# Kernel tuning notes

Measured on AMD Instinct MI355X. Metric: run time of the kernel, lower is better.

## Reference

```python
import jax, jax.numpy as jnp
import numpy as np
from jax import lax

EMB_DIM = 16
NUM_EMB = 32
DN = ('NCDHW', 'OIDHW', 'NCDHW')


def conv3d(x, w, b, stride, pad):
    y = lax.conv_general_dilated(x, w, window_strides=(stride,) * 3,
                                 padding=[(pad, pad)] * 3, dimension_numbers=DN)
    return y + b[None, :, None, None, None]


def deconv3d(x, w, b, stride, pad):
    # PyTorch ConvTranspose3d: weight (Cin,Cout,k,k,k); equivalent to conv with
    # spatially flipped, channel-transposed kernel, lhs_dilation=stride, pad=k-1-p.
    k = w.shape[-1]
    wf = jnp.flip(w, axis=(2, 3, 4)).transpose(1, 0, 2, 3, 4)  # (Cout,Cin,k,k,k)
    y = lax.conv_general_dilated(x, wf, window_strides=(1, 1, 1),
                                 padding=[(k - 1 - pad, k - 1 - pad)] * 3,
                                 lhs_dilation=(stride,) * 3, dimension_numbers=DN)
    return y + b[None, :, None, None, None]


def setup_inputs() -> dict:
    key = jax.random.key(0)
    ks = jax.random.split(key, 16)
    x = jax.random.normal(ks[0], (16, 3, 16, 128, 128), dtype=jnp.float32)
    s = 0.05
    # encoder params
    enc_w1 = jax.random.normal(ks[1], (4, 3, 4, 4, 4), jnp.float32) * s
    enc_b1 = jnp.zeros((4,), jnp.float32)
    enc_w2 = jax.random.normal(ks[2], (8, 4, 4, 4, 4), jnp.float32) * s
    enc_b2 = jnp.zeros((8,), jnp.float32)
    enc_w4 = jax.random.normal(ks[3], (EMB_DIM, 8, 3, 3, 3), jnp.float32) * s
    enc_b4 = jnp.zeros((EMB_DIM,), jnp.float32)
    # decoder params (ConvTranspose3d layout: (Cin, Cout, k, k, k))
    dec_w1 = jax.random.normal(ks[4], (EMB_DIM, 8, 4, 4, 4), jnp.float32) * s
    dec_b1 = jnp.zeros((8,), jnp.float32)
    dec_w3 = jax.random.normal(ks[5], (8, 4, 4, 4, 4), jnp.float32) * s
    dec_b3 = jnp.zeros((4,), jnp.float32)
    dec_w4 = jax.random.normal(ks[6], (4, 3, 3, 3, 3), jnp.float32) * s
    dec_b4 = jnp.zeros((3,), jnp.float32)
    # codebook buffers: normalize(randn)*0.1, rows 0/1 forced
    e = jax.random.normal(ks[7], (NUM_EMB, EMB_DIM), jnp.float32)
    e = e / jnp.linalg.norm(e, axis=1, keepdims=True) * 0.1
    embedding = e.at[0].set(0.0).at[1].set(6.0)
    cluster_size = jnp.ones((NUM_EMB,), jnp.float32)
    return dict(x=x, epoch=60,
                enc_w1=enc_w1, enc_b1=enc_b1, enc_w2=enc_w2, enc_b2=enc_b2,
                enc_w4=enc_w4, enc_b4=enc_b4,
                dec_w1=dec_w1, dec_b1=dec_b1, dec_w3=dec_w3, dec_b3=dec_b3,
                dec_w4=dec_w4, dec_b4=dec_b4,
                embedding=embedding, cluster_size=cluster_size)


def reference(x, epoch, enc_w1, enc_b1, enc_w2, enc_b2, enc_w4, enc_b4,
              dec_w1, dec_b1, dec_w3, dec_b3, dec_w4, dec_b4,
              embedding, cluster_size):
    # ---- Encoder ----
    h = jax.nn.relu(conv3d(x, enc_w1, enc_b1, 2, 1))
    h = jax.nn.relu(conv3d(h, enc_w2, enc_b2, 2, 1))
    z = jnp.clip(conv3d(h, enc_w4, enc_b4, 1, 1), 0.0, 6.0)  # relu(relu6(.))
    B, C, Dd, Hh, Ww = z.shape

    # ---- VQ-EMA forward (epoch >= 50 branch) ----
    emb = embedding.at[0].set(0.0).at[1].set(6.0)
    flat = z.transpose(0, 2, 3, 4, 1).reshape(-1, C)  # (N, D)
    # squared euclidean distances; argmin matches cdist argmin
    d2 = (jnp.sum(flat * flat, axis=1, keepdims=True)
          - 2.0 * flat @ emb.T + jnp.sum(emb * emb, axis=1))
    idx = jnp.argmin(d2, axis=1)                       # (N,)
    q = emb[idx]                                       # (N, D)
    quant = q.reshape(B, Dd, Hh, Ww, C).transpose(0, 4, 1, 2, 3)

    N = flat.shape[0]
    avg_probs = jnp.zeros((NUM_EMB,), flat.dtype).at[idx].add(1.0) / N
    perplexity = jnp.exp(-jnp.sum(avg_probs * jnp.log(avg_probs + 1e-10)))
    used_codes = jnp.sum(cluster_size > 1e-5).astype(jnp.float32) / NUM_EMB

    quantized_st = z + lax.stop_gradient(quant - z)
    vq_loss = 0.25 * jnp.mean((lax.stop_gradient(quant) - z) ** 2)
    codes = idx.reshape(B, Dd, Hh, Ww)

    # ---- Decoder ----
    d = jax.nn.relu(deconv3d(quantized_st, dec_w1, dec_b1, 2, 1))
    d = jax.nn.relu(deconv3d(d, dec_w3, dec_b3, 2, 1))
    out = deconv3d(d, dec_w4, dec_b4, 1, 1)
    return out, vq_loss, codes, perplexity, used_codes
```

## Files before the change

kernel.cpp:

```cpp
#include <hip/hip_runtime.h>
#include <math.h>

#define NB 16


__device__ __forceinline__ float4 ld4(const float* p) {
  return *reinterpret_cast<const float4*>(p);
}
__device__ __forceinline__ void st4(float* p, float4 v) {
  *reinterpret_cast<float4*>(p) = v;
}

__global__ __launch_bounds__(256) void conv1_k(
    const float* __restrict__ x, const float* __restrict__ w,
    const float* __restrict__ bias, float* __restrict__ y) {
  int idx = blockIdx.x * 256 + threadIdx.x;
  int g  = idx & 15;
  int oh = (idx >> 4) & 63;
  int od = (idx >> 10) & 7;
  int n  = idx >> 13;
  bool gl = (g > 0), gr = (g < 15);
  float acc[4][4];
  #pragma unroll
  for (int co = 0; co < 4; co++) {
    float bv = bias[co];
    #pragma unroll
    for (int m = 0; m < 4; m++) acc[co][m] = bv;
  }
  int ih0 = 2 * oh - 1;
  #pragma unroll 1
  for (int ci = 0; ci < 3; ci++) {
    #pragma unroll 1
    for (int kd = 0; kd < 4; kd++) {
      int id = 2 * od - 1 + kd;
      bool vd = (unsigned)id < 16u;
      int idc = vd ? id : 0;
      const float* plane = x + (((n * 3 + ci) * 16 + idc) * 16384);
      #pragma unroll
      for (int kh = 0; kh < 4; kh++) {
        int ih = ih0 + kh;
        bool v = vd && ((unsigned)ih < 128u);
        int ihc = (unsigned)ih < 128u ? ih : 0;
        const float* rp = plane + ihc * 128 + 8 * g;
        float r[10];
        float4 A = ld4(rp);
        float4 B = ld4(rp + 4);
        float rl = rp[-1 * (int)gl];
        float rr = rp[gr ? 8 : 0];
        r[0] = (v && gl) ? rl : 0.0f;
        r[1] = v ? A.x : 0.0f; r[2] = v ? A.y : 0.0f;
        r[3] = v ? A.z : 0.0f; r[4] = v ? A.w : 0.0f;
        r[5] = v ? B.x : 0.0f; r[6] = v ? B.y : 0.0f;
        r[7] = v ? B.z : 0.0f; r[8] = v ? B.w : 0.0f;
        r[9] = (v && gr) ? rr : 0.0f;
        #pragma unroll
        for (int co = 0; co < 4; co++) {
          const float* wb = w + ((co * 3 + ci) * 4 + kd) * 16 + kh * 4;
          #pragma unroll
          for (int kw = 0; kw < 4; kw++) {
            float wv = wb[kw];
            #pragma unroll
            for (int m = 0; m < 4; m++)
              acc[co][m] += r[2 * m + kw] * wv;
          }
        }
      }
    }
  }
  #pragma unroll
  for (int co = 0; co < 4; co++) {
    float4 o;
    o.x = fmaxf(acc[co][0], 0.0f); o.y = fmaxf(acc[co][1], 0.0f);
    o.z = fmaxf(acc[co][2], 0.0f); o.w = fmaxf(acc[co][3], 0.0f);
    st4(y + ((n * 4 + co) * 8 + od) * 4096 + oh * 64 + 4 * g, o);
  }
}

__global__ __launch_bounds__(256) void conv2_k(
    const float* __restrict__ y1, const float* __restrict__ w,
    const float* __restrict__ bias, float* __restrict__ y) {
  int idx = blockIdx.x * 256 + threadIdx.x;
  int ow = idx & 31;
  int oh = (idx >> 5) & 31;
  int od = (idx >> 10) & 3;
  int n = (idx >> 12) & 15;
  int cog = idx >> 16;
  float acc[4];
  #pragma unroll
  for (int co = 0; co < 4; co++) acc[co] = bias[cog * 4 + co];
  int id0 = 2 * od - 1, ih0 = 2 * oh - 1, iw0 = 2 * ow - 1;
  bool vh[4], vw[4];
  #pragma unroll
  for (int l = 0; l < 4; l++) {
    vh[l] = (unsigned)(ih0 + l) < 64u;
    vw[l] = (unsigned)(iw0 + l) < 64u;
  }
  #pragma unroll 1
  for (int ci = 0; ci < 4; ci++) {
    const float* ip = y1 + ((n * 4 + ci) * 8) * 4096;
    #pragma unroll
    for (int kd = 0; kd < 4; kd++) {
      int id = id0 + kd;
      bool vd = (unsigned)id < 8u;
      const float* pp = ip + id * 4096;
      float p[4][4];
      #pragma unroll
      for (int kh = 0; kh < 4; kh++)
        #pragma unroll
        for (int kw = 0; kw < 4; kw++)
          p[kh][kw] = (vd && vh[kh] && vw[kw]) ? pp[(ih0 + kh) * 64 + (iw0 + kw)] : 0.0f;
      #pragma unroll
      for (int co = 0; co < 4; co++) {
        const float* wp = w + (((cog * 4 + co) * 4 + ci) * 4 + kd) * 16;
        #pragma unroll
        for (int kh = 0; kh < 4; kh++)
          #pragma unroll
          for (int kw = 0; kw < 4; kw++)
            acc[co] += p[kh][kw] * wp[kh * 4 + kw];
      }
    }
  }
  #pragma unroll
  for (int co = 0; co < 4; co++)
    y[((n * 8 + cog * 4 + co) * 4 + od) * 1024 + oh * 32 + ow] = fmaxf(acc[co], 0.0f);
}

__global__ __launch_bounds__(256) void conv4_k(
    const float* __restrict__ y2, const float* __restrict__ w,
    const float* __restrict__ bias, float* __restrict__ z) {
  int idx = blockIdx.x * 256 + threadIdx.x;
  int ow = idx & 31;
  int oh = (idx >> 5) & 31;
  int od = (idx >> 10) & 3;
  int n = (idx >> 12) & 15;
  int cog = idx >> 16;
  float acc[4];
  #pragma unroll
  for (int co = 0; co < 4; co++) acc[co] = bias[cog * 4 + co];
  bool vh[3], vw[3];
  #pragma unroll
  for (int l = 0; l < 3; l++) {
    vh[l] = (unsigned)(oh - 1 + l) < 32u;
    vw[l] = (unsigned)(ow - 1 + l) < 32u;
  }
  #pragma unroll 1
  for (int ci = 0; ci < 8; ci++) {
    const float* ip = y2 + ((n * 8 + ci) * 4) * 1024;
    #pragma unroll
    for (int kd = 0; kd < 3; kd++) {
      int id = od - 1 + kd;
      bool vd = (unsigned)id < 4u;
      const float* pp = ip + id * 1024;
      float p[3][3];
      #pragma unroll
      for (int kh = 0; kh < 3; kh++)
        #pragma unroll
        for (int kw = 0; kw < 3; kw++)
          p[kh][kw] = (vd && vh[kh] && vw[kw]) ? pp[(oh - 1 + kh) * 32 + (ow - 1 + kw)] : 0.0f;
      #pragma unroll
      for (int co = 0; co < 4; co++) {
        const float* wp = w + (((cog * 4 + co) * 8 + ci) * 3 + kd) * 9;
        #pragma unroll
        for (int kh = 0; kh < 3; kh++)
          #pragma unroll
          for (int kw = 0; kw < 3; kw++)
            acc[co] += p[kh][kw] * wp[kh * 3 + kw];
      }
    }
  }
  #pragma unroll
  for (int co = 0; co < 4; co++)
    z[((n * 16 + cog * 4 + co) * 4 + od) * 1024 + oh * 32 + ow] =
        fminf(fmaxf(acc[co], 0.0f), 6.0f);
}

__global__ __launch_bounds__(256) void vq_k(
    const float* __restrict__ z, const float* __restrict__ emb,
    float* __restrict__ quant, float* __restrict__ codes_out,
    float* __restrict__ stats) {
  __shared__ float se[32 * 16];
  __shared__ float se2[32];
  __shared__ float shist[32];
  __shared__ float swred[4];
  int tid = threadIdx.x;
  for (int i = tid; i < 512; i += 256) {
    int r = i >> 4;
    float v = emb[i];
    if (r == 0) v = 0.0f;
    else if (r == 1) v = 6.0f;
    se[i] = v;
  }
  if (tid < 32) shist[tid] = 0.0f;
  __syncthreads();
  if (tid < 32) {
    float s = 0.0f;
    #pragma unroll
    for (int d = 0; d < 16; d++) { float v = se[tid * 16 + d]; s += v * v; }
    se2[tid] = s;
  }
  __syncthreads();

  int idx = blockIdx.x * 256 + tid;
  float lsum = 0.0f;
  {
    int w_ = idx & 31; int t = idx >> 5;
    int h_ = t & 31; t >>= 5;
    int d_ = t & 3;  int b_ = t >> 2;
    const float* zp = z + b_ * 65536 + d_ * 1024 + h_ * 32 + w_;
    float f[16];
    float f2 = 0.0f;
    #pragma unroll
    for (int c = 0; c < 16; c++) { float v = zp[c * 4096]; f[c] = v; f2 += v * v; }
    float best = 1e30f; int bi = 0;
    for (int e = 0; e < 32; e++) {
      float dot = 0.0f;
      #pragma unroll
      for (int c = 0; c < 16; c++) dot += f[c] * se[e * 16 + c];
      float d2 = f2 - 2.0f * dot + se2[e];
      if (d2 < best) { best = d2; bi = e; }
    }
    float* qp = quant + b_ * 65536 + d_ * 1024 + h_ * 32 + w_;
    #pragma unroll
    for (int c = 0; c < 16; c++) {
      float q = se[bi * 16 + c];
      qp[c * 4096] = q;
      float df = q - f[c];
      lsum += df * df;
    }
    codes_out[idx] = (float)bi;
    atomicAdd(&shist[bi], 1.0f);
  }
  for (int o = 32; o; o >>= 1) lsum += __shfl_down(lsum, o);
  if ((tid & 63) == 0) swred[tid >> 6] = lsum;
  __syncthreads();
  if (tid == 0) atomicAdd(&stats[0], swred[0] + swred[1] + swred[2] + swred[3]);
  if (tid < 32) {
    float h = shist[tid];
    if (h != 0.0f) atomicAdd(&stats[1 + tid], h);
  }
}

__global__ void init_stats_k(float* __restrict__ stats) {
  int tid = threadIdx.x;
  if (tid < 33) stats[tid] = 0.0f;
}

__global__ void fin_k(const float* __restrict__ stats,
                      const float* __restrict__ cluster_size,
                      float* __restrict__ out_loss, float* __restrict__ out_perp,
                      float* __restrict__ out_used) {
  int tid = threadIdx.x;
  float v = 0.0f;
  float used = 0.0f;
  if (tid < 32) {
    float p = stats[1 + tid] * (1.0f / 65536.0f);
    v = p * logf(p + 1e-10f);
    used = (cluster_size[tid] > 1e-5f) ? 1.0f : 0.0f;
  }
  for (int o = 16; o; o >>= 1) { v += __shfl_down(v, o); used += __shfl_down(used, o); }
  if (tid == 0) {
    *out_perp = expf(-v);
    *out_used = used * (1.0f / 32.0f);
    *out_loss = 0.25f * stats[0] * (1.0f / 1048576.0f);
  }
}

__global__ __launch_bounds__(256) void deconv1_k(
    const float* __restrict__ q, const float* __restrict__ w,
    const float* __restrict__ bias, float* __restrict__ d1) {
  int bid = blockIdx.x;
  int cog = bid & 1;
  int ph  = (bid >> 1) & 1;
  int od  = (bid >> 2) & 7;
  int n   = bid >> 5;
  int tid = threadIdx.x;
  int g   = tid & 7;
  int bl  = tid >> 3;
  bool glf = (g > 0), grf = (g < 7);

  int kd0 = (od + 1) & 1;
  int idtop = (od + 1 - kd0) >> 1;
  int kh0 = (ph + 1) & 1;
  int ihtop = bl + ph;

  float acc[4][8];
  #pragma unroll
  for (int co = 0; co < 4; co++) {
    float bv = bias[cog * 4 + co];
    #pragma unroll
    for (int m = 0; m < 8; m++) acc[co][m] = bv;
  }

  #pragma unroll 1
  for (int ci = 0; ci < 16; ci++) {
    const float* ip = q + ((n * 16 + ci) * 4) * 1024;
    #pragma unroll
    for (int jd = 0; jd < 2; jd++) {
      int id = idtop - jd;
      bool vd = (unsigned)id < 4u;
      int idc = vd ? id : 0;
      const float* plane = ip + idc * 1024;
      #pragma unroll
      for (int jh = 0; jh < 2; jh++) {
        int ih = ihtop - jh;
        bool v = vd && ((unsigned)ih < 32u);
        int ihc = (unsigned)ih < 32u ? ih : 0;
        const float* rp = plane + ihc * 32 + 4 * g;
        float r[6];
        float4 A = ld4(rp);
        float rl = rp[-1 * (int)glf];
        float rr = rp[grf ? 4 : 0];
        r[0] = (v && glf) ? rl : 0.0f;
        r[1] = v ? A.x : 0.0f; r[2] = v ? A.y : 0.0f;
        r[3] = v ? A.z : 0.0f; r[4] = v ? A.w : 0.0f;
        r[5] = (v && grf) ? rr : 0.0f;
        int kd = kd0 + 2 * jd;
        int kh = kh0 + 2 * jh;
        #pragma unroll
        for (int co = 0; co < 4; co++) {
          const float* wb = w + ((ci * 8 + cog * 4 + co) * 4 + kd) * 16 + kh * 4;
          #pragma unroll
          for (int jw = 0; jw < 2; jw++) {
            float w_ev = wb[1 + 2 * jw];
            float w_od = wb[2 * jw];
            #pragma unroll
            for (int ii = 0; ii < 4; ii++) {
              acc[co][2 * ii]     += r[ii + 1 - jw] * w_ev;
              acc[co][2 * ii + 1] += r[ii + 2 - jw] * w_od;
            }
          }
        }
      }
    }
  }
  int oh = 2 * bl + ph;
  #pragma unroll
  for (int co = 0; co < 4; co++) {
    float* op = d1 + ((n * 8 + cog * 4 + co) * 8 + od) * 4096 + oh * 64 + 8 * g;
    float4 lo, hi;
    lo.x = fmaxf(acc[co][0], 0.0f); lo.y = fmaxf(acc[co][1], 0.0f);
    lo.z = fmaxf(acc[co][2], 0.0f); lo.w = fmaxf(acc[co][3], 0.0f);
    hi.x = fmaxf(acc[co][4], 0.0f); hi.y = fmaxf(acc[co][5], 0.0f);
    hi.z = fmaxf(acc[co][6], 0.0f); hi.w = fmaxf(acc[co][7], 0.0f);
    st4(op, lo); st4(op + 4, hi);
  }
}

__global__ __launch_bounds__(256) void deconv3_k(
    const float* __restrict__ d1, const float* __restrict__ w,
    const float* __restrict__ bias, float* __restrict__ d2) {
  int bid = blockIdx.x;
  int ph  = bid & 1;
  int blh = (bid >> 1) & 3;
  int od  = (bid >> 3) & 15;
  int n   = bid >> 7;
  int tid = threadIdx.x;
  int g   = tid & 15;
  int bl  = tid >> 4;
  int BL  = blh * 16 + bl;
  bool glf = (g > 0), grf = (g < 15);

  int kd0 = (od + 1) & 1;
  int idtop = (od + 1 - kd0) >> 1;
  int kh0 = (ph + 1) & 1;
  int ihtop = BL + ph;

  float acc[4][8];
  #pragma unroll
  for (int co = 0; co < 4; co++) {
    float bv = bias[co];
    #pragma unroll
    for (int m = 0; m < 8; m++) acc[co][m] = bv;
  }

  #pragma unroll 1
  for (int ci = 0; ci < 8; ci++) {
    const float* ip = d1 + ((n * 8 + ci) * 8) * 4096;
    #pragma unroll
    for (int jd = 0; jd < 2; jd++) {
      int id = idtop - jd;
      bool vd = (unsigned)id < 8u;
      int idc = vd ? id : 0;
      const float* plane = ip + idc * 4096;
      #pragma unroll
      for (int jh = 0; jh < 2; jh++) {
        int ih = ihtop - jh;
        bool v = vd && ((unsigned)ih < 64u);
        int ihc = (unsigned)ih < 64u ? ih : 0;
        const float* rp = plane + ihc * 64 + 4 * g;
        float r[6];
        float4 A = ld4(rp);
        float rl = rp[-1 * (int)glf];
        float rr = rp[grf ? 4 : 0];
        r[0] = (v && glf) ? rl : 0.0f;
        r[1] = v ? A.x : 0.0f; r[2] = v ? A.y : 0.0f;
        r[3] = v ? A.z : 0.0f; r[4] = v ? A.w : 0.0f;
        r[5] = (v && grf) ? rr : 0.0f;
        int kd = kd0 + 2 * jd;
        int kh = kh0 + 2 * jh;
        #pragma unroll
        for (int co = 0; co < 4; co++) {
          const float* wb = w + ((ci * 4 + co) * 4 + kd) * 16 + kh * 4;
          #pragma unroll
          for (int jw = 0; jw < 2; jw++) {
            float w_ev = wb[1 + 2 * jw];
            float w_od = wb[2 * jw];
            #pragma unroll
            for (int ii = 0; ii < 4; ii++) {
              acc[co][2 * ii]     += r[ii + 1 - jw] * w_ev;
              acc[co][2 * ii + 1] += r[ii + 2 - jw] * w_od;
            }
          }
        }
      }
    }
  }
  int oh = 2 * BL + ph;
  #pragma unroll
  for (int co = 0; co < 4; co++) {
    float* op = d2 + ((n * 4 + co) * 16 + od) * 16384 + oh * 128 + 8 * g;
    float4 lo, hi;
    lo.x = fmaxf(acc[co][0], 0.0f); lo.y = fmaxf(acc[co][1], 0.0f);
    lo.z = fmaxf(acc[co][2], 0.0f); lo.w = fmaxf(acc[co][3], 0.0f);
    hi.x = fmaxf(acc[co][4], 0.0f); hi.y = fmaxf(acc[co][5], 0.0f);
    hi.z = fmaxf(acc[co][6], 0.0f); hi.w = fmaxf(acc[co][7], 0.0f);
    st4(op, lo); st4(op + 4, hi);
  }
}

__global__ __launch_bounds__(256) void deconv4_k(
    const float* __restrict__ d2, const float* __restrict__ w,
    const float* __restrict__ bias, float* __restrict__ out) {
  int idx = blockIdx.x * 256 + threadIdx.x;
  int g  = idx & 15;
  int oh = (idx >> 4) & 127;
  int od = (idx >> 11) & 15;
  int n  = idx >> 15;
  bool gl = (g > 0), gr = (g < 15);
  float acc[3][8];
  #pragma unroll
  for (int co = 0; co < 3; co++) {
    float bv = bias[co];
    #pragma unroll
    for (int m = 0; m < 8; m++) acc[co][m] = bv;
  }
  int ih0 = oh - 1;
  #pragma unroll 1
  for (int ci = 0; ci < 4; ci++) {
    const float* ip = d2 + ((n * 4 + ci) * 16) * 16384;
    #pragma unroll
    for (int kd = 0; kd < 3; kd++) {
      int id = od - 1 + kd;
      bool vd = (unsigned)id < 16u;
      int idc = vd ? id : 0;
      const float* plane = ip + idc * 16384;
      #pragma unroll
      for (int kh = 0; kh < 3; kh++) {
        int ih = ih0 + kh;
        bool v = vd && ((unsigned)ih < 128u);
        int ihc = (unsigned)ih < 128u ? ih : 0;
        const float* rp = plane + ihc * 128 + 8 * g;
        float r[10];
        float4 A = ld4(rp);
        float4 B = ld4(rp + 4);
        float rl = rp[-1 * (int)gl];
        float rr = rp[gr ? 8 : 0];
        r[0] = (v && gl) ? rl : 0.0f;
        r[1] = v ? A.x : 0.0f; r[2] = v ? A.y : 0.0f;
        r[3] = v ? A.z : 0.0f; r[4] = v ? A.w : 0.0f;
        r[5] = v ? B.x : 0.0f; r[6] = v ? B.y : 0.0f;
        r[7] = v ? B.z : 0.0f; r[8] = v ? B.w : 0.0f;
        r[9] = (v && gr) ? rr : 0.0f;
        #pragma unroll
        for (int co = 0; co < 3; co++) {
          const float* wb = w + (ci * 3 + co) * 27 + (2 - kd) * 9 + (2 - kh) * 3 + 2;
          #pragma unroll
          for (int kw = 0; kw < 3; kw++) {
            float wv = wb[-kw];
            #pragma unroll
            for (int m = 0; m < 8; m++)
              acc[co][m] += r[m + kw] * wv;
          }
        }
      }
    }
  }
  #pragma unroll
  for (int co = 0; co < 3; co++) {
    float* op = out + ((n * 3 + co) * 16 + od) * 16384 + oh * 128 + 8 * g;
    float4 lo, hi;
    lo.x = acc[co][0]; lo.y = acc[co][1]; lo.z = acc[co][2]; lo.w = acc[co][3];
    hi.x = acc[co][4]; hi.y = acc[co][5]; hi.z = acc[co][6]; hi.w = acc[co][7];
    st4(op, lo); st4(op + 4, hi);
  }
}

extern "C" void kernel_launch(void* const* d_in, const int* in_sizes, int n_in,
                              void* d_out, int out_size, void* d_ws, size_t ws_size,
                              hipStream_t stream) {
  const float* x      = (const float*)d_in[0];
  const float* enc_w1 = (const float*)d_in[2];
  const float* enc_b1 = (const float*)d_in[3];
  const float* enc_w2 = (const float*)d_in[4];
  const float* enc_b2 = (const float*)d_in[5];
  const float* enc_w4 = (const float*)d_in[6];
  const float* enc_b4 = (const float*)d_in[7];
  const float* dec_w1 = (const float*)d_in[8];
  const float* dec_b1 = (const float*)d_in[9];
  const float* dec_w3 = (const float*)d_in[10];
  const float* dec_b3 = (const float*)d_in[11];
  const float* dec_w4 = (const float*)d_in[12];
  const float* dec_b4 = (const float*)d_in[13];
  const float* emb    = (const float*)d_in[14];
  const float* csize  = (const float*)d_in[15];

  float* ws = (float*)d_ws;
  float* stats = ws;
  float* quant = ws + 64;
  float* z     = quant + 1048576;
  float* y2    = z + 1048576;
  float* y1    = y2 + 524288;
  float* d1    = z;
  float* d2    = ws + 64 + 1048576 + 4194304;

  float* out   = (float*)d_out;
  float* out_loss  = out + 12582912;
  float* out_codes = out_loss + 1;
  float* out_perp  = out_codes + 65536;
  float* out_used  = out_perp + 1;

  init_stats_k<<<1, 64, 0, stream>>>(stats);

  conv1_k<<<512, 256, 0, stream>>>(x, enc_w1, enc_b1, y1);
  conv2_k<<<512, 256, 0, stream>>>(y1, enc_w2, enc_b2, y2);
  conv4_k<<<1024, 256, 0, stream>>>(y2, enc_w4, enc_b4, z);

  vq_k<<<256, 256, 0, stream>>>(z, emb, quant, out_codes, stats);
  fin_k<<<1, 64, 0, stream>>>(stats, csize, out_loss, out_perp, out_used);

  deconv1_k<<<512, 256, 0, stream>>>(quant, dec_w1, dec_b1, d1);
  deconv3_k<<<2048, 256, 0, stream>>>(d1, dec_w3, dec_b3, d2);
  deconv4_k<<<2048, 256, 0, stream>>>(d2, dec_w4, dec_b4, out);
}
```

Before: 399.2 us.

## Retile final 3x3x3 conv as 2x2x2 output cubes per thread

The last decoder conv kernel changes from each thread computing an 8-wide row strip to computing a 2x2x2 output cube, loading a 4x4x4 input patch of scalar values per input channel. The aim is more input reuse in all three dimensions instead of only along width, which cuts global and cache loads per output. In exchange, loads and stores become scalar and strided (stride-2 store pattern within a warp), so coalescing is worse and register use for the patch and accumulators is higher.

After: 371.6 us. 6.9% less time.

```diff
diff --git a/kernel.cpp b/kernel.cpp
--- a/kernel.cpp
+++ b/kernel.cpp
@@ -432,67 +432,70 @@
     const float* __restrict__ d2, const float* __restrict__ w,
     const float* __restrict__ bias, float* __restrict__ out) {
   int idx = blockIdx.x * 256 + threadIdx.x;
-  int g  = idx & 15;
-  int oh = (idx >> 4) & 127;
-  int od = (idx >> 11) & 15;
-  int n  = idx >> 15;
-  bool gl = (g > 0), gr = (g < 15);
-  float acc[3][8];
-  #pragma unroll
-  for (int co = 0; co < 3; co++) {
-    float bv = bias[co];
-    #pragma unroll
-    for (int m = 0; m < 8; m++) acc[co][m] = bv;
-  }
-  int ih0 = oh - 1;
+  int c = idx & 63;
+  int b = (idx >> 6) & 63;
+  int a = (idx >> 12) & 7;
+  int n = idx >> 15;
+  float acc[2][2][2][3];
+  #pragma unroll
+  for (int pd = 0; pd < 2; pd++)
+    #pragma unroll
+    for (int ph = 0; ph < 2; ph++)
+      #pragma unroll
+      for (int pw = 0; pw < 2; pw++)
+        #pragma unroll
+        for (int co = 0; co < 3; co++) acc[pd][ph][pw][co] = bias[co];
+  int ih0 = 2 * b - 1, iw0 = 2 * c - 1;
+  bool vh[4], vw[4];
+  #pragma unroll
+  for (int l = 0; l < 4; l++) {
+    vh[l] = (unsigned)(ih0 + l) < 128u;
+    vw[l] = (unsigned)(iw0 + l) < 128u;
+  }
   #pragma unroll 1
   for (int ci = 0; ci < 4; ci++) {
     const float* ip = d2 + ((n * 4 + ci) * 16) * 16384;
     #pragma unroll
-    for (int kd = 0; kd < 3; kd++) {
-      int id = od - 1 + kd;
-      bool vd = (unsigned)id < 16u;
-      int idc = vd ? id : 0;
-      const float* plane = ip + idc * 16384;
-      #pragma unroll
-      for (int kh = 0; kh < 3; kh++) {
-        int ih = ih0 + kh;
-        bool v = vd && ((unsigned)ih < 128u);
-        int ihc = (unsigned)ih < 128u ? ih : 0;
-        const float* rp = plane + ihc * 128 + 8 * g;
-        float r[10];
-        float4 A = ld4(rp);
-        float4 B = ld4(rp + 4);
-        float rl = rp[-1 * (int)gl];
-        float rr = rp[gr ? 8 : 0];
-        r[0] = (v && gl) ? rl : 0.0f;
-        r[1] = v ? A.x : 0.0f; r[2] = v ? A.y : 0.0f;
-        r[3] = v ? A.z : 0.0f; r[4] = v ? A.w : 0.0f;
-        r[5] = v ? B.x : 0.0f; r[6] = v ? B.y : 0.0f;
-        r[7] = v ? B.z : 0.0f; r[8] = v ? B.w : 0.0f;
-        r[9] = (v && gr) ? rr : 0.0f;
-        #pragma unroll
-        for (int co = 0; co < 3; co++) {
-          const float* wb = w + (ci * 3 + co) * 27 + (2 - kd) * 9 + (2 - kh) * 3 + 2;
+    for (int ld = 0; ld < 4; ld++) {
+      int id = 2 * a - 1 + ld;
+      bool vdl = (unsigned)id < 16u;
+      const float* pp = ip + id * 16384;
+      float p[4][4];
+      #pragma unroll
+      for (int lh = 0; lh < 4; lh++)
+        #pragma unroll
+        for (int lw = 0; lw < 4; lw++)
+          p[lh][lw] = (vdl && vh[lh] && vw[lw]) ? pp[(ih0 + lh) * 128 + (iw0 + lw)] : 0.0f;
+      #pragma unroll
+      for (int pd = 0; pd < 2; pd++) {
+        int kd = pd + 2 - ld;
+        if (kd < 0 || kd > 2) continue;
+        #pragma unroll
+        for (int kh = 0; kh < 3; kh++)
           #pragma unroll
-          for (int kw = 0; kw < 3; kw++) {
-            float wv = wb[-kw];
+          for (int kw = 0; kw < 3; kw++)
             #pragma unroll
-            for (int m = 0; m < 8; m++)
-              acc[co][m] += r[m + kw] * wv;
-          }
-        }
+            for (int co = 0; co < 3; co++) {
+              float wv = w[(ci * 3 + co) * 27 + kd * 9 + kh * 3 + kw];
+              #pragma unroll
+              for (int ph = 0; ph < 2; ph++)
+                #pragma unroll
+                for (int pw = 0; pw < 2; pw++)
+                  acc[pd][ph][pw][co] += p[ph + 2 - kh][pw + 2 - kw] * wv;
+            }
       }
     }
   }
   #pragma unroll
-  for (int co = 0; co < 3; co++) {
-    float* op = out + ((n * 3 + co) * 16 + od) * 16384 + oh * 128 + 8 * g;
-    float4 lo, hi;
-    lo.x = acc[co][0]; lo.y = acc[co][1]; lo.z = acc[co][2]; lo.w = acc[co][3];
-    hi.x = acc[co][4]; hi.y = acc[co][5]; hi.z = acc[co][6]; hi.w = acc[co][7];
-    st4(op, lo); st4(op + 4, hi);
-  }
+  for (int co = 0; co < 3; co++)
+    #pragma unroll
+    for (int pd = 0; pd < 2; pd++)
+      #pragma unroll
+      for (int ph = 0; ph < 2; ph++)
+        #pragma unroll
+        for (int pw = 0; pw < 2; pw++)
+          out[((n * 3 + co) * 16 + 2 * a + pd) * 16384 +
+              (2 * b + ph) * 128 + (2 * c + pw)] = acc[pd][ph][pw][co];
 }
 
 extern "C" void kernel_launch(void* const* d_in, const int* in_sizes, int n_in,
```

## Tile final deconv through shared memory with zero-padded halo and 16-wide outputs

Applied to the files above, without the earlier changes.

The last 3x3x3 transposed conv now stages each input plane tile (34 rows by 130 columns, zero-padded) in LDS per (kd, ci). Each thread computes 16 outputs per row instead of 8, with half as many blocks launched. The goal is to cut redundant global loads and the per-element boundary masking. In exchange it adds syncthreads barriers, an integer-divide index calculation in the load loop, and more registers for the accumulators, which may lower occupancy.

Result: slower. 421.3 us (+5.5%).

```diff
diff --git a/kernel.cpp b/kernel.cpp
--- a/kernel.cpp
+++ b/kernel.cpp
@@ -428,70 +428,92 @@
   }
 }
 
+#define D4_STRIDE 140
+#define D4_ELEMS (34 * D4_STRIDE)
 __global__ __launch_bounds__(256) void deconv4_k(
     const float* __restrict__ d2, const float* __restrict__ w,
     const float* __restrict__ bias, float* __restrict__ out) {
-  int idx = blockIdx.x * 256 + threadIdx.x;
-  int g  = idx & 15;
-  int oh = (idx >> 4) & 127;
-  int od = (idx >> 11) & 15;
-  int n  = idx >> 15;
-  bool gl = (g > 0), gr = (g < 15);
-  float acc[3][8];
+  __shared__ float sh[D4_ELEMS];
+  int bid = blockIdx.x;
+  int ohg = bid & 3;
+  int od  = (bid >> 2) & 15;
+  int n   = bid >> 6;
+  int tid = threadIdx.x;
+  int owg = tid & 7;
+  int ohl = tid >> 3;
+  int ow0 = 16 * owg;
+  int oh0m1 = 32 * ohg - 1;
+
+  float acc[3][16];
   #pragma unroll
   for (int co = 0; co < 3; co++) {
     float bv = bias[co];
     #pragma unroll
-    for (int m = 0; m < 8; m++) acc[co][m] = bv;
-  }
-  int ih0 = oh - 1;
+    for (int m = 0; m < 16; m++) acc[co][m] = bv;
+  }
+
   #pragma unroll 1
-  for (int ci = 0; ci < 4; ci++) {
-    const float* ip = d2 + ((n * 4 + ci) * 16) * 16384;
-    #pragma unroll
-    for (int kd = 0; kd < 3; kd++) {
-      int id = od - 1 + kd;
-      bool vd = (unsigned)id < 16u;
-      int idc = vd ? id : 0;
-      const float* plane = ip + idc * 16384;
+  for (int kd = 0; kd < 3; kd++) {
+    int id = od - 1 + kd;
+    if ((unsigned)id >= 16u) continue;
+    #pragma unroll 1
+    for (int ci = 0; ci < 4; ci++) {
+      const float* gp = d2 + ((n * 4 + ci) * 16 + id) * 16384;
+      __syncthreads();
+      #pragma unroll 1
+      for (int k = 0; k < 19; k++) {
+        int e = tid + k * 256;
+        if (e < D4_ELEMS) {
+          int row = e / D4_STRIDE;
+          int lcol = e - row * D4_STRIDE;
+          int ih = oh0m1 + row;
+          int iw = lcol - 1;
+          float v = 0.0f;
+          if (lcol < 130 && (unsigned)ih < 128u && (unsigned)iw < 128u)
+            v = gp[ih * 128 + iw];
+          sh[e] = v;
+        }
+      }
+      __syncthreads();
       #pragma unroll
       for (int kh = 0; kh < 3; kh++) {
-        int ih = ih0 + kh;
-        bool v = vd && ((unsigned)ih < 128u);
-        int ihc = (unsigned)ih < 128u ? ih : 0;
-        const float* rp = plane + ihc * 128 + 8 * g;
-        float r[10];
+        const float* rp = &sh[(ohl + kh) * D4_STRIDE + ow0];
+        float r[18];
         float4 A = ld4(rp);
         float4 B = ld4(rp + 4);
-        float rl = rp[-1 * (int)gl];
-        float rr = rp[gr ? 8 : 0];
-        r[0] = (v && gl) ? rl : 0.0f;
-        r[1] = v ? A.x : 0.0f; r[2] = v ? A.y : 0.0f;
-        r[3] = v ? A.z : 0.0f; r[4] = v ? A.w : 0.0f;
-        r[5] = v ? B.x : 0.0f; r[6] = v ? B.y : 0.0f;
-        r[7] = v ? B.z : 0.0f; r[8] = v ? B.w : 0.0f;
-        r[9] = (v && gr) ? rr : 0.0f;
+        float4 C = ld4(rp + 8);
+        float4 D = ld4(rp + 12);
+        r[0] = A.x;  r[1] = A.y;  r[2] = A.z;  r[3] = A.w;
+        r[4] = B.x;  r[5] = B.y;  r[6] = B.z;  r[7] = B.w;
+        r[8] = C.x;  r[9] = C.y;  r[10] = C.z; r[11] = C.w;
+        r[12] = D.x; r[13] = D.y; r[14] = D.z; r[15] = D.w;
+        r[16] = rp[16]; r[17] = rp[17];
         #pragma unroll
         for (int co = 0; co < 3; co++) {
-          const float* wb = w + (ci * 3 + co) * 27 + (2 - kd) * 9 + (2 - kh) * 3 + 2;
+          const float* wb = w + (ci * 3 + co) * 27 + (2 - kd) * 9 + (2 - kh) * 3;
           #pragma unroll
           for (int kw = 0; kw < 3; kw++) {
-            float wv = wb[-kw];
+            float wv = wb[2 - kw];
             #pragma unroll
-            for (int m = 0; m < 8; m++)
+            for (int m = 0; m < 16; m++)
               acc[co][m] += r[m + kw] * wv;
           }
         }
       }
     }
   }
+
+  int oh = 32 * ohg + ohl;
   #pragma unroll
   for (int co = 0; co < 3; co++) {
-    float* op = out + ((n * 3 + co) * 16 + od) * 16384 + oh * 128 + 8 * g;
-    float4 lo, hi;
-    lo.x = acc[co][0]; lo.y = acc[co][1]; lo.z = acc[co][2]; lo.w = acc[co][3];
-    hi.x = acc[co][4]; hi.y = acc[co][5]; hi.z = acc[co][6]; hi.w = acc[co][7];
-    st4(op, lo); st4(op + 4, hi);
+    float* op = out + ((n * 3 + co) * 16 + od) * 16384 + oh * 128 + ow0;
+    #pragma unroll
+    for (int q = 0; q < 4; q++) {
+      float4 o;
+      o.x = acc[co][4 * q]; o.y = acc[co][4 * q + 1];
+      o.z = acc[co][4 * q + 2]; o.w = acc[co][4 * q + 3];
+      st4(op + 4 * q, o);
+    }
   }
 }
 
@@ -540,5 +562,5 @@
 
   deconv1_k<<<512, 256, 0, stream>>>(quant, dec_w1, dec_b1, d1);
   deconv3_k<<<2048, 256, 0, stream>>>(d1, dec_w3, dec_b3, d2);
-  deconv4_k<<<2048, 256, 0, stream>>>(d2, dec_w4, dec_b4, out);
-}
+  deconv4_k<<<1024, 256, 0, stream>>>(d2, dec_w4, dec_b4, out);
+}
```
